# Kernel optimization log

Measured on AMD Instinct MI355X. Metric: run time of the kernel, lower is better.

Reference implementation:

```python
import jax, jax.numpy as jnp
import numpy as np

N = 100000        # nodes
E = 1600000       # edges
G = 128           # graphs in batch
D_FEAT = 240      # continuous node features (input_features - 1)
EMB = 16          # node-type embedding dim
H = 256           # hidden size (both layers)
PH = 128          # pool / classifier hidden
GF = 32           # global feature dim
LN_EPS = 1e-5


def setup_inputs() -> dict:
    key = jax.random.key(0)
    ks = jax.random.split(key, 24)

    node_types = jax.random.randint(ks[0], (N,), 0, 400).astype(jnp.float32)
    feats = jax.random.normal(ks[1], (N, D_FEAT), dtype=jnp.float32)
    x = jnp.concatenate([node_types[:, None], feats], axis=1)  # [N, 241]

    edge_index = jax.random.randint(ks[2], (2, E), 0, N, dtype=jnp.int32)
    batch = jnp.sort(jax.random.randint(ks[3], (N,), 0, G, dtype=jnp.int32))
    global_features = jax.random.normal(ks[4], (G, GF), dtype=jnp.float32)

    s = 0.05
    p = {}
    p['emb_table'] = jax.random.normal(ks[5], (400, EMB), dtype=jnp.float32) * s
    # layer 0 GIN MLP (in=256 -> 256 -> 256) + LayerNorm
    p['l0_w1'] = jax.random.normal(ks[6], (H, H), dtype=jnp.float32) * s
    p['l0_b1'] = jnp.zeros((H,), jnp.float32)
    p['l0_w2'] = jax.random.normal(ks[7], (H, H), dtype=jnp.float32) * s
    p['l0_b2'] = jnp.zeros((H,), jnp.float32)
    p['ln0_g'] = jnp.ones((H,), jnp.float32)
    p['ln0_b'] = jnp.zeros((H,), jnp.float32)
    # layer 1
    p['l1_w1'] = jax.random.normal(ks[8], (H, H), dtype=jnp.float32) * s
    p['l1_b1'] = jnp.zeros((H,), jnp.float32)
    p['l1_w2'] = jax.random.normal(ks[9], (H, H), dtype=jnp.float32) * s
    p['l1_b2'] = jnp.zeros((H,), jnp.float32)
    p['ln1_g'] = jnp.ones((H,), jnp.float32)
    p['ln1_b'] = jnp.zeros((H,), jnp.float32)
    # attentional aggregation gate: 256 -> 128 -> 1
    p['gate_w1'] = jax.random.normal(ks[10], (H, PH), dtype=jnp.float32) * s
    p['gate_b1'] = jnp.zeros((PH,), jnp.float32)
    p['gate_w2'] = jax.random.normal(ks[11], (PH, 1), dtype=jnp.float32) * s
    p['gate_b2'] = jnp.zeros((1,), jnp.float32)
    # classifier: 256+32 -> 128 -> 2
    p['cls_w1'] = jax.random.normal(ks[12], (H + GF, PH), dtype=jnp.float32) * s
    p['cls_b1'] = jnp.zeros((PH,), jnp.float32)
    p['cls_w2'] = jax.random.normal(ks[13], (PH, 2), dtype=jnp.float32) * s
    p['cls_b2'] = jnp.zeros((2,), jnp.float32)

    return dict(x=x, edge_index=edge_index, batch=batch,
                global_features=global_features, **p)


def _layernorm(z, g, b):
    mu = jnp.mean(z, axis=-1, keepdims=True)
    var = jnp.mean(jnp.square(z - mu), axis=-1, keepdims=True)
    return (z - mu) * jax.lax.rsqrt(var + LN_EPS) * g + b


def _gin_block(h, src, dst, w1, b1, w2, b2, ln_g, ln_b):
    # GINConv, eps=0: mlp((1+eps)*x_i + sum_{j->i} x_j)
    agg = jax.ops.segment_sum(h[src], dst, num_segments=h.shape[0])
    z = h + agg
    z = jax.nn.relu(z @ w1 + b1) @ w2 + b2
    z = jax.nn.relu(_layernorm(z, ln_g, ln_b))
    return h + z  # dropout is identity in eval; residual


def reference(x, edge_index, batch, global_features, emb_table,
              l0_w1, l0_b1, l0_w2, l0_b2, ln0_g, ln0_b,
              l1_w1, l1_b1, l1_w2, l1_b2, ln1_g, ln1_b,
              gate_w1, gate_b1, gate_w2, gate_b2,
              cls_w1, cls_b1, cls_w2, cls_b2):
    node_types = x[:, 0].astype(jnp.int32)
    h = jnp.concatenate([x[:, 1:], emb_table[node_types]], axis=1)  # [N, 256]

    src, dst = edge_index[0], edge_index[1]
    h = _gin_block(h, src, dst, l0_w1, l0_b1, l0_w2, l0_b2, ln0_g, ln0_b)
    h = _gin_block(h, src, dst, l1_w1, l1_b1, l1_w2, l1_b2, ln1_g, ln1_b)

    # AttentionalAggregation: segment softmax over gate scores, weighted sum
    gate = jax.nn.relu(h @ gate_w1 + gate_b1) @ gate_w2 + gate_b2  # [N, 1]
    gate = gate[:, 0]
    m = jax.ops.segment_max(gate, batch, num_segments=G)
    a = jnp.exp(gate - m[batch])
    s = jax.ops.segment_sum(a, batch, num_segments=G)
    w = a / s[batch]
    pooled = jax.ops.segment_sum(w[:, None] * h, batch, num_segments=G)  # [G, 256]

    z = jnp.concatenate([pooled, global_features], axis=1)  # [G, 288]
    out = jax.nn.relu(z @ cls_w1 + cls_b1) @ cls_w2 + cls_b2  # [G, 2]
    return out
```

## Files before the change

### kernel.cpp

```cpp
#include <hip/hip_runtime.h>
#include <math.h>

#define N_NODES 100000
#define N_EDGES 1600000
#define NG      128
#define HD      256
#define PHD     128
#define GFD     32
#define XW      241
#define LN_EPS  1e-5f
#define SLOT    64

typedef __attribute__((ext_vector_type(8))) short bf8_t;
typedef __attribute__((ext_vector_type(4))) float f4_t;

static __device__ __forceinline__ float relu_f(float x){ return fmaxf(x, 0.0f); }

static __device__ __forceinline__ unsigned short f2bf_rn(float v) {
    unsigned int u = __float_as_uint(v);
    unsigned int r = (u + 0x7fffu + ((u >> 16) & 1u)) >> 16;
    return (unsigned short)r;
}
static __device__ __forceinline__ float bf2f(unsigned short h) {
    return __uint_as_float((unsigned int)h << 16);
}

__global__ void build_h_kernel(const float* __restrict__ x, const float* __restrict__ emb,
                               float* __restrict__ h, unsigned short* __restrict__ h16)
{
    int node = blockIdx.x;
    int tid  = threadIdx.x;
    const float* xr = x + (size_t)node * XW;
    float v;
    if (tid < 240) {
        v = xr[1 + tid];
    } else {
        int t = (int)xr[0];
        v = emb[t * 16 + (tid - 240)];
    }
    h[(size_t)node * HD + tid] = v;
    h16[(size_t)node * HD + tid] = f2bf_rn(v);
}

__global__ void fill_slots_kernel(const int* __restrict__ src, const int* __restrict__ dst,
                                  int* __restrict__ cnt, int* __restrict__ col, int e)
{
    int i = blockIdx.x * blockDim.x + threadIdx.x;
    if (i < e) {
        int d = dst[i];
        int p = atomicAdd(&cnt[d], 1);
        if (p < SLOT) col[(size_t)d * SLOT + p] = src[i];
    }
}

static __device__ __forceinline__ void pack_one(const float* __restrict__ w, short* __restrict__ hi,
                                                int N, int fbase)
{
    int lane = threadIdx.x & 63;
    int f = fbase * 4 + (threadIdx.x >> 6);
    const int KB = 8;
    int nb = f / KB, kb = f % KB;
    int n = nb * 16 + (lane & 15);
    int k0 = kb * 32 + (lane >> 4) * 8;
    size_t o = (size_t)f * 512 + lane * 8;
    #pragma unroll
    for (int j = 0; j < 8; j++) {
        float v = w[(size_t)(k0 + j) * N + n];
        hi[o + j] = (short)f2bf_rn(v);
    }
}

__global__ __launch_bounds__(256) void pack_all_kernel(
    const float* __restrict__ w0, const float* __restrict__ w1,
    const float* __restrict__ w2, const float* __restrict__ w3,
    const float* __restrict__ w4,
    short* o0h, short* o1h, short* o2h, short* o3h, short* o4h)
{
    int b = blockIdx.x;
    if      (b < 32)  pack_one(w0, o0h, HD,  b);
    else if (b < 64)  pack_one(w1, o1h, HD,  b - 32);
    else if (b < 96)  pack_one(w2, o2h, HD,  b - 64);
    else if (b < 128) pack_one(w3, o3h, HD,  b - 96);
    else              pack_one(w4, o4h, PHD, b - 128);
}

static __device__ __forceinline__ void mm32(
    f4_t (&acc)[2][4], const char* buf,
    const short* __restrict__ Bh,
    int wc, int cb, int kg, int lane)
{
    bf8_t bcur[4], bnxt[4];
    #pragma unroll
    for (int ni = 0; ni < 4; ni++)
        bcur[ni] = *(const bf8_t*)&Bh[((size_t)((wc*4+ni)*8))*512 + lane*8];
    for (int kb = 0; kb < 8; kb++) {
        if (kb < 7) {
            #pragma unroll
            for (int ni = 0; ni < 4; ni++)
                bnxt[ni] = *(const bf8_t*)&Bh[((size_t)((wc*4+ni)*8 + kb+1))*512 + lane*8];
        }
        bf8_t ahi[2], alo[2];
        #pragma unroll
        for (int mi = 0; mi < 2; mi++) {
            int row = mi*16 + cb;
            int byte = (row*512 + kb*64 + kg*16) ^ ((row & 7) << 4);
            ahi[mi] = *(const bf8_t*)(buf + byte);
            alo[mi] = *(const bf8_t*)(buf + 16384 + byte);
        }
        #pragma unroll
        for (int mi = 0; mi < 2; mi++)
            #pragma unroll
            for (int ni = 0; ni < 4; ni++)
                acc[mi][ni] = __builtin_amdgcn_mfma_f32_16x16x32_bf16(ahi[mi], bcur[ni], acc[mi][ni], 0, 0, 0);
        #pragma unroll
        for (int mi = 0; mi < 2; mi++)
            #pragma unroll
            for (int ni = 0; ni < 4; ni++)
                acc[mi][ni] = __builtin_amdgcn_mfma_f32_16x16x32_bf16(alo[mi], bcur[ni], acc[mi][ni], 0, 0, 0);
        #pragma unroll
        for (int ni = 0; ni < 4; ni++) bcur[ni] = bnxt[ni];
    }
}

__global__ __launch_bounds__(256, 4) void gin_layer_kernel(
    float* __restrict__ h, const unsigned short* __restrict__ h16i,
    unsigned short* __restrict__ h16o,
    const int* __restrict__ cnt, const int* __restrict__ col,
    const short* __restrict__ w1h, const float* __restrict__ b1,
    const short* __restrict__ w2h, const float* __restrict__ b2,
    const float* __restrict__ lng, const float* __restrict__ lnb)
{
    __shared__ char buf[32768];
    const int tid  = threadIdx.x;
    const int lane = tid & 63;
    const int wv   = tid >> 6;
    const int cb   = lane & 15;
    const int kg   = lane >> 4;
    const int l4   = lane * 4;
    const long row0 = (long)blockIdx.x * 32;

    for (int rr = 0; rr < 8; rr++) {
        int row = wv * 8 + rr;
        long grow = row0 + row;
        float4 a0 = *(const float4*)&h[grow * HD + l4];
        float4 a1 = make_float4(0,0,0,0), a2 = make_float4(0,0,0,0), a3 = make_float4(0,0,0,0);
        int deg = cnt[grow]; if (deg > SLOT) deg = SLOT;
        const int* cb4 = col + (size_t)grow * SLOT;
        int e = 0;
        for (; e + 4 <= deg; e += 4) {
            int s0 = cb4[e], s1 = cb4[e+1], s2 = cb4[e+2], s3 = cb4[e+3];
            ushort4 u0 = *(const ushort4*)&h16i[(size_t)s0 * HD + l4];
            ushort4 u1 = *(const ushort4*)&h16i[(size_t)s1 * HD + l4];
            ushort4 u2 = *(const ushort4*)&h16i[(size_t)s2 * HD + l4];
            ushort4 u3 = *(const ushort4*)&h16i[(size_t)s3 * HD + l4];
            a0.x += bf2f(u0.x); a0.y += bf2f(u0.y); a0.z += bf2f(u0.z); a0.w += bf2f(u0.w);
            a1.x += bf2f(u1.x); a1.y += bf2f(u1.y); a1.z += bf2f(u1.z); a1.w += bf2f(u1.w);
            a2.x += bf2f(u2.x); a2.y += bf2f(u2.y); a2.z += bf2f(u2.z); a2.w += bf2f(u2.w);
            a3.x += bf2f(u3.x); a3.y += bf2f(u3.y); a3.z += bf2f(u3.z); a3.w += bf2f(u3.w);
        }
        for (; e < deg; e++) {
            int s = cb4[e];
            ushort4 u = *(const ushort4*)&h16i[(size_t)s * HD + l4];
            a0.x += bf2f(u.x); a0.y += bf2f(u.y); a0.z += bf2f(u.z); a0.w += bf2f(u.w);
        }
        a0.x += a1.x + a2.x + a3.x;
        a0.y += a1.y + a2.y + a3.y;
        a0.z += a1.z + a2.z + a3.z;
        a0.w += a1.w + a2.w + a3.w;
        ushort4 hi4, lo4;
        unsigned short hb;
        hb = f2bf_rn(a0.x); hi4.x = hb; lo4.x = f2bf_rn(a0.x - bf2f(hb));
        hb = f2bf_rn(a0.y); hi4.y = hb; lo4.y = f2bf_rn(a0.y - bf2f(hb));
        hb = f2bf_rn(a0.z); hi4.z = hb; lo4.z = f2bf_rn(a0.z - bf2f(hb));
        hb = f2bf_rn(a0.w); hi4.w = hb; lo4.w = f2bf_rn(a0.w - bf2f(hb));
        int byte = (row * 512 + lane * 8) ^ ((row & 7) << 4);
        *(ushort4*)(buf + byte)         = hi4;
        *(ushort4*)(buf + 16384 + byte) = lo4;
    }
    __syncthreads();

    f4_t acc[2][4];
    const f4_t zero4 = {0.f, 0.f, 0.f, 0.f};
    #pragma unroll
    for (int mi = 0; mi < 2; mi++)
        #pragma unroll
        for (int ni = 0; ni < 4; ni++) acc[mi][ni] = zero4;

    mm32(acc, buf, w1h, wv, cb, kg, lane);
    __syncthreads();

    {
        float bias1[4];
        #pragma unroll
        for (int ni = 0; ni < 4; ni++) bias1[ni] = b1[wv * 64 + ni * 16 + cb];
        #pragma unroll
        for (int mi = 0; mi < 2; mi++) {
            #pragma unroll
            for (int ni = 0; ni < 4; ni++) {
                int colx2 = (wv * 64 + ni * 16 + cb) * 2;
                #pragma unroll
                for (int j = 0; j < 4; j++) {
                    float t = relu_f(acc[mi][ni][j] + bias1[ni]);
                    int row = mi * 16 + kg * 4 + j;
                    unsigned short hb = f2bf_rn(t);
                    unsigned short lb = f2bf_rn(t - bf2f(hb));
                    int byte = (row * 512 + colx2) ^ ((row & 7) << 4);
                    *(short*)(buf + byte)         = (short)hb;
                    *(short*)(buf + 16384 + byte) = (short)lb;
                }
            }
        }
    }
    __syncthreads();

    #pragma unroll
    for (int mi = 0; mi < 2; mi++)
        #pragma unroll
        for (int ni = 0; ni < 4; ni++) acc[mi][ni] = zero4;

    mm32(acc, buf, w2h, wv, cb, kg, lane);
    __syncthreads();

    {
        float bias2[4];
        #pragma unroll
        for (int ni = 0; ni < 4; ni++) bias2[ni] = b2[wv * 64 + ni * 16 + cb];
        #pragma unroll
        for (int mi = 0; mi < 2; mi++) {
            #pragma unroll
            for (int ni = 0; ni < 4; ni++) {
                int col2 = wv * 64 + ni * 16 + cb;
                #pragma unroll
                for (int j = 0; j < 4; j++) {
                    int row = mi * 16 + kg * 4 + j;
                    int byte = (row * 1024 + col2 * 4) ^ (((row >> 2) & 3) << 6);
                    *(float*)(buf + byte) = acc[mi][ni][j] + bias2[ni];
                }
            }
        }
    }
    __syncthreads();

    {
        const float4 gv = *(const float4*)&lng[l4];
        const float4 bv = *(const float4*)&lnb[l4];
        for (int rr = 0; rr < 8; rr++) {
            int row = wv * 8 + rr;
            long grow = row0 + row;
            int byte = (row * 1024 + lane * 16) ^ (((row >> 2) & 3) << 6);
            float4 v = *(const float4*)(buf + byte);
            float s = v.x + v.y + v.z + v.w;
            float q = v.x * v.x + v.y * v.y + v.z * v.z + v.w * v.w;
            #pragma unroll
            for (int off = 32; off > 0; off >>= 1) {
                s += __shfl_xor(s, off, 64);
                q += __shfl_xor(q, off, 64);
            }
            float mu = s * (1.0f / 256.0f);
            float var = q * (1.0f / 256.0f) - mu * mu;
            float rstd = rsqrtf(var + LN_EPS);
            size_t gi = (size_t)grow * HD + l4;
            float4 hv = *(float4*)&h[gi];
            hv.x += relu_f((v.x - mu) * rstd * gv.x + bv.x);
            hv.y += relu_f((v.y - mu) * rstd * gv.y + bv.y);
            hv.z += relu_f((v.z - mu) * rstd * gv.z + bv.z);
            hv.w += relu_f((v.w - mu) * rstd * gv.w + bv.w);
            *(float4*)&h[gi] = hv;
            ushort4 m16;
            m16.x = f2bf_rn(hv.x); m16.y = f2bf_rn(hv.y);
            m16.z = f2bf_rn(hv.z); m16.w = f2bf_rn(hv.w);
            *(ushort4*)&h16o[gi] = m16;
        }
    }
}

__global__ __launch_bounds__(256, 2) void gate_mfma_kernel(
    const float* __restrict__ h,
    const short* __restrict__ g1h, const float* __restrict__ gb1,
    const float* __restrict__ gw2, const float* __restrict__ gb2,
    float* __restrict__ gate)
{
    __shared__ char buf[65536];
    const int tid  = threadIdx.x;
    const int lane = tid & 63;
    const int wv   = tid >> 6;
    const int cb   = lane & 15;
    const int kg   = lane >> 4;
    const long row0 = (long)blockIdx.x * 64;

    for (int rr = 0; rr < 16; rr++) {
        int row = wv * 16 + rr;
        long grow = row0 + row;
        float4 v = make_float4(0.f, 0.f, 0.f, 0.f);
        if (grow < N_NODES) v = *(const float4*)&h[grow * HD + lane * 4];
        ushort4 hi4, lo4;
        unsigned short hb;
        hb = f2bf_rn(v.x); hi4.x = hb; lo4.x = f2bf_rn(v.x - bf2f(hb));
        hb = f2bf_rn(v.y); hi4.y = hb; lo4.y = f2bf_rn(v.y - bf2f(hb));
        hb = f2bf_rn(v.z); hi4.z = hb; lo4.z = f2bf_rn(v.z - bf2f(hb));
        hb = f2bf_rn(v.w); hi4.w = hb; lo4.w = f2bf_rn(v.w - bf2f(hb));
        int byte = (row * 512 + lane * 8) ^ ((row & 7) << 4);
        *(ushort4*)(buf + byte)         = hi4;
        *(ushort4*)(buf + 32768 + byte) = lo4;
    }
    __syncthreads();

    f4_t acc[4][2];
    const f4_t zero4 = {0.f, 0.f, 0.f, 0.f};
    #pragma unroll
    for (int mi = 0; mi < 4; mi++) { acc[mi][0] = zero4; acc[mi][1] = zero4; }

    #pragma unroll
    for (int pass = 0; pass < 2; pass++) {
        const char* Abase = (pass == 1) ? (buf + 32768) : buf;
        for (int kb = 0; kb < 8; kb++) {
            bf8_t a[4], b[2];
            #pragma unroll
            for (int mi = 0; mi < 4; mi++) {
                int row = mi * 16 + cb;
                int byte = (row * 512 + kb * 64 + kg * 16) ^ ((row & 7) << 4);
                a[mi] = *(const bf8_t*)(Abase + byte);
            }
            #pragma unroll
            for (int ni = 0; ni < 2; ni++) {
                int nb = wv * 2 + ni;
                b[ni] = *(const bf8_t*)&g1h[(size_t)(nb * 8 + kb) * 512 + lane * 8];
            }
            #pragma unroll
            for (int mi = 0; mi < 4; mi++)
                #pragma unroll
                for (int ni = 0; ni < 2; ni++)
                    acc[mi][ni] = __builtin_amdgcn_mfma_f32_16x16x32_bf16(a[mi], b[ni], acc[mi][ni], 0, 0, 0);
        }
    }
    __syncthreads();

    {
        float* G1 = (float*)buf;
        float bias1[2];
        bias1[0] = gb1[wv * 32 + cb];
        bias1[1] = gb1[wv * 32 + 16 + cb];
        #pragma unroll
        for (int mi = 0; mi < 4; mi++) {
            #pragma unroll
            for (int ni = 0; ni < 2; ni++) {
                int colv = wv * 32 + ni * 16 + cb;
                #pragma unroll
                for (int j = 0; j < 4; j++) {
                    int row = mi * 16 + kg * 4 + j;
                    G1[row * PHD + colv] = relu_f(acc[mi][ni][j] + bias1[ni]);
                }
            }
        }
    }
    __syncthreads();

    {
        const float* G1 = (const float*)buf;
        float2 wv2 = *(const float2*)&gw2[lane * 2];
        float b2v = gb2[0];
        for (int rr = 0; rr < 16; rr++) {
            int row = wv * 16 + rr;
            long grow = row0 + row;
            if (grow >= N_NODES) break;
            float2 t2 = *(const float2*)&G1[row * PHD + lane * 2];
            float p = t2.x * wv2.x + t2.y * wv2.y;
            #pragma unroll
            for (int off = 32; off > 0; off >>= 1) p += __shfl_xor(p, off, 64);
            if (lane == 0) gate[grow] = p + b2v;
        }
    }
}

__global__ void goff_kernel(const int* __restrict__ batch, int* __restrict__ goff, int n)
{
    int t = threadIdx.x;
    if (t > NG) return;
    int lo = 0, hi = n;
    while (lo < hi) {
        int mid = (lo + hi) >> 1;
        if (batch[mid] < t) lo = mid + 1; else hi = mid;
    }
    goff[t] = lo;
}

__global__ __launch_bounds__(256) void pool_kernel(
    const float* __restrict__ h, const float* __restrict__ gate,
    const int* __restrict__ goff, float* __restrict__ pooled)
{
    __shared__ float red[256];
    __shared__ float m_sh, s_sh;
    int g = blockIdx.x >> 2, q = blockIdx.x & 3;
    int tid = threadIdx.x;
    int beg = goff[g], end = goff[g + 1];
    if (beg >= end) return;

    float lm = -3.4e38f;
    for (int i = beg + tid; i < end; i += 256) lm = fmaxf(lm, gate[i]);
    red[tid] = lm; __syncthreads();
    for (int off = 128; off > 0; off >>= 1) {
        if (tid < off) red[tid] = fmaxf(red[tid], red[tid + off]);
        __syncthreads();
    }
    if (tid == 0) m_sh = red[0];
    __syncthreads();
    float m = m_sh;

    float ls = 0.0f;
    for (int i = beg + tid; i < end; i += 256) ls += expf(gate[i] - m);
    __syncthreads();
    red[tid] = ls; __syncthreads();
    for (int off = 128; off > 0; off >>= 1) {
        if (tid < off) red[tid] += red[tid + off];
        __syncthreads();
    }
    if (tid == 0) s_sh = red[0];
    __syncthreads();
    float inv_s = 1.0f / s_sh;

    float acc = 0.0f;
    for (int i = beg + q; i < end; i += 4) {
        float a = expf(gate[i] - m);
        acc += a * h[(size_t)i * HD + tid];
    }
    atomicAdd(&pooled[(size_t)g * HD + tid], acc * inv_s);
}

__global__ __launch_bounds__(128) void cls_kernel(
    const float* __restrict__ pooled, const float* __restrict__ gf,
    const float* __restrict__ w1, const float* __restrict__ b1,
    const float* __restrict__ w2, const float* __restrict__ b2,
    float* __restrict__ out)
{
    __shared__ float r0[128], r1[128];
    int g = blockIdx.x, c = threadIdx.x;
    float acc = b1[c];
    const float* pr = pooled + (size_t)g * HD;
    for (int k = 0; k < HD; k++) acc += pr[k] * w1[k * PHD + c];
    const float* gr = gf + g * GFD;
    for (int k = 0; k < GFD; k++) acc += gr[k] * w1[(HD + k) * PHD + c];
    float t = relu_f(acc);
    r0[c] = t * w2[c * 2 + 0];
    r1[c] = t * w2[c * 2 + 1];
    __syncthreads();
    for (int off = 64; off > 0; off >>= 1) {
        if (c < off) { r0[c] += r0[c + off]; r1[c] += r1[c + off]; }
        __syncthreads();
    }
    if (c == 0) {
        out[g * 2 + 0] = r0[0] + b2[0];
        out[g * 2 + 1] = r1[0] + b2[1];
    }
}

extern "C" void kernel_launch(void* const* d_in, const int* in_sizes, int n_in,
                              void* d_out, int out_size, void* d_ws, size_t ws_size,
                              hipStream_t stream)
{
    const float* x    = (const float*)d_in[0];
    const int*   ei   = (const int*)d_in[1];
    const int*   bat  = (const int*)d_in[2];
    const float* gf   = (const float*)d_in[3];
    const float* emb  = (const float*)d_in[4];
    const float* l0w1 = (const float*)d_in[5];
    const float* l0b1 = (const float*)d_in[6];
    const float* l0w2 = (const float*)d_in[7];
    const float* l0b2 = (const float*)d_in[8];
    const float* ln0g = (const float*)d_in[9];
    const float* ln0b = (const float*)d_in[10];
    const float* l1w1 = (const float*)d_in[11];
    const float* l1b1 = (const float*)d_in[12];
    const float* l1w2 = (const float*)d_in[13];
    const float* l1b2 = (const float*)d_in[14];
    const float* ln1g = (const float*)d_in[15];
    const float* ln1b = (const float*)d_in[16];
    const float* gw1  = (const float*)d_in[17];
    const float* gb1  = (const float*)d_in[18];
    const float* gw2  = (const float*)d_in[19];
    const float* gb2  = (const float*)d_in[20];
    const float* cw1  = (const float*)d_in[21];
    const float* cb1  = (const float*)d_in[22];
    const float* cw2  = (const float*)d_in[23];
    const float* cb2  = (const float*)d_in[24];

    char* ws = (char*)d_ws;
    size_t off = 0;
    auto alloc = [&](size_t bytes) {
        void* p = ws + off;
        off += (bytes + 255) & ~(size_t)255;
        return p;
    };
    float* h      = (float*)alloc((size_t)N_NODES * HD * 4);
    unsigned short* h16a = (unsigned short*)alloc((size_t)N_NODES * HD * 2);
    unsigned short* h16b = (unsigned short*)alloc((size_t)N_NODES * HD * 2);
    float* gate   = (float*)alloc((size_t)N_NODES * 4);
    int*   cnt    = (int*)alloc((size_t)N_NODES * 4);
    int*   col    = (int*)alloc((size_t)N_NODES * SLOT * 4);
    int*   goff   = (int*)alloc((NG + 1) * 4);
    float* pooled = (float*)alloc((size_t)NG * HD * 4);
    short* p_l0w1h = (short*)alloc((size_t)HD * HD * 2);
    short* p_l0w2h = (short*)alloc((size_t)HD * HD * 2);
    short* p_l1w1h = (short*)alloc((size_t)HD * HD * 2);
    short* p_l1w2h = (short*)alloc((size_t)HD * HD * 2);
    short* p_gw1h  = (short*)alloc((size_t)HD * PHD * 2);

    const int* src = ei;
    const int* dst = ei + N_EDGES;

    build_h_kernel<<<N_NODES, 256, 0, stream>>>(x, emb, h, h16a);

    hipMemsetAsync(cnt, 0, (size_t)N_NODES * 4, stream);
    fill_slots_kernel<<<(N_EDGES + 255) / 256, 256, 0, stream>>>(src, dst, cnt, col, N_EDGES);

    pack_all_kernel<<<144, 256, 0, stream>>>(l0w1, l0w2, l1w1, l1w2, gw1,
                                             p_l0w1h, p_l0w2h, p_l1w1h, p_l1w2h, p_gw1h);

    const int layer_grid = N_NODES / 32;

    gin_layer_kernel<<<layer_grid, 256, 0, stream>>>(h, h16a, h16b, cnt, col,
                                                     p_l0w1h, l0b1, p_l0w2h, l0b2, ln0g, ln0b);
    gin_layer_kernel<<<layer_grid, 256, 0, stream>>>(h, h16b, h16a, cnt, col,
                                                     p_l1w1h, l1b1, p_l1w2h, l1b2, ln1g, ln1b);

    gate_mfma_kernel<<<(N_NODES + 63) / 64, 256, 0, stream>>>(h, p_gw1h, gb1, gw2, gb2, gate);
    goff_kernel<<<1, 256, 0, stream>>>(bat, goff, N_NODES);
    hipMemsetAsync(pooled, 0, (size_t)NG * HD * 4, stream);
    pool_kernel<<<NG * 4, 256, 0, stream>>>(h, gate, goff, pooled);
    cls_kernel<<<NG, 128, 0, stream>>>(pooled, gf, cw1, cb1, cw2, cb2, (float*)d_out);
}
```

Baseline: 769.7 us.

## Merge prep kernels into one launch and use bf16 single-pass gate GEMM

Three setup kernels (edge slot filling, input h construction, weight packing) are merged into one prep kernel whose block ranges pick the task, removing launch gaps. The col writes now use nontemporal stores. The gate kernel reads the already-available bf16 copy of h and drops the hi/lo split-bf16 second MFMA pass, halving gate GEMM work and the fp32 h read. This lowers gate-score precision to plain bf16, which may affect tolerance.

```diff
diff --git a/kernel.cpp b/kernel.cpp
--- a/kernel.cpp
+++ b/kernel.cpp
@@ -10,6 +10,8 @@
 #define XW      241
 #define LN_EPS  1e-5f
 #define SLOT    64
+#define EDGE_NB ((N_EDGES + 255) / 256)
+#define PACK_NB 144
 
 typedef __attribute__((ext_vector_type(8))) short bf8_t;
 typedef __attribute__((ext_vector_type(4))) float f4_t;
@@ -23,34 +25,6 @@
 }
 static __device__ __forceinline__ float bf2f(unsigned short h) {
     return __uint_as_float((unsigned int)h << 16);
-}
-
-__global__ void build_h_kernel(const float* __restrict__ x, const float* __restrict__ emb,
-                               float* __restrict__ h, unsigned short* __restrict__ h16)
-{
-    int node = blockIdx.x;
-    int tid  = threadIdx.x;
-    const float* xr = x + (size_t)node * XW;
-    float v;
-    if (tid < 240) {
-        v = xr[1 + tid];
-    } else {
-        int t = (int)xr[0];
-        v = emb[t * 16 + (tid - 240)];
-    }
-    h[(size_t)node * HD + tid] = v;
-    h16[(size_t)node * HD + tid] = f2bf_rn(v);
-}
-
-__global__ void fill_slots_kernel(const int* __restrict__ src, const int* __restrict__ dst,
-                                  int* __restrict__ cnt, int* __restrict__ col, int e)
-{
-    int i = blockIdx.x * blockDim.x + threadIdx.x;
-    if (i < e) {
-        int d = dst[i];
-        int p = atomicAdd(&cnt[d], 1);
-        if (p < SLOT) col[(size_t)d * SLOT + p] = src[i];
-    }
 }
 
 static __device__ __forceinline__ void pack_one(const float* __restrict__ w, short* __restrict__ hi,
@@ -70,18 +44,45 @@
     }
 }
 
-__global__ __launch_bounds__(256) void pack_all_kernel(
+__global__ __launch_bounds__(256) void prep_kernel(
+    const float* __restrict__ x, const float* __restrict__ emb,
+    float* __restrict__ h, unsigned short* __restrict__ h16,
+    const int* __restrict__ src, const int* __restrict__ dst,
+    int* __restrict__ cnt, int* __restrict__ col,
     const float* __restrict__ w0, const float* __restrict__ w1,
     const float* __restrict__ w2, const float* __restrict__ w3,
     const float* __restrict__ w4,
     short* o0h, short* o1h, short* o2h, short* o3h, short* o4h)
 {
     int b = blockIdx.x;
-    if      (b < 32)  pack_one(w0, o0h, HD,  b);
-    else if (b < 64)  pack_one(w1, o1h, HD,  b - 32);
-    else if (b < 96)  pack_one(w2, o2h, HD,  b - 64);
-    else if (b < 128) pack_one(w3, o3h, HD,  b - 96);
-    else              pack_one(w4, o4h, PHD, b - 128);
+    int tid = threadIdx.x;
+    if (b < EDGE_NB) {
+        int i = b * 256 + tid;
+        if (i < N_EDGES) {
+            int d = dst[i];
+            int p = atomicAdd(&cnt[d], 1);
+            if (p < SLOT) __builtin_nontemporal_store(src[i], &col[(size_t)d * SLOT + p]);
+        }
+    } else if (b < EDGE_NB + N_NODES) {
+        int node = b - EDGE_NB;
+        const float* xr = x + (size_t)node * XW;
+        float v;
+        if (tid < 240) {
+            v = xr[1 + tid];
+        } else {
+            int t = (int)xr[0];
+            v = emb[t * 16 + (tid - 240)];
+        }
+        h[(size_t)node * HD + tid] = v;
+        h16[(size_t)node * HD + tid] = f2bf_rn(v);
+    } else {
+        int bb = b - EDGE_NB - N_NODES;
+        if      (bb < 32)  pack_one(w0, o0h, HD,  bb);
+        else if (bb < 64)  pack_one(w1, o1h, HD,  bb - 32);
+        else if (bb < 96)  pack_one(w2, o2h, HD,  bb - 64);
+        else if (bb < 128) pack_one(w3, o3h, HD,  bb - 96);
+        else               pack_one(w4, o4h, PHD, bb - 128);
+    }
 }
 
 static __device__ __forceinline__ void mm32(
@@ -275,7 +276,7 @@
 }
 
 __global__ __launch_bounds__(256, 2) void gate_mfma_kernel(
-    const float* __restrict__ h,
+    const unsigned short* __restrict__ h16,
     const short* __restrict__ g1h, const float* __restrict__ gb1,
     const float* __restrict__ gw2, const float* __restrict__ gb2,
     float* __restrict__ gate)
@@ -291,17 +292,10 @@
     for (int rr = 0; rr < 16; rr++) {
         int row = wv * 16 + rr;
         long grow = row0 + row;
-        float4 v = make_float4(0.f, 0.f, 0.f, 0.f);
-        if (grow < N_NODES) v = *(const float4*)&h[grow * HD + lane * 4];
-        ushort4 hi4, lo4;
-        unsigned short hb;
-        hb = f2bf_rn(v.x); hi4.x = hb; lo4.x = f2bf_rn(v.x - bf2f(hb));
-        hb = f2bf_rn(v.y); hi4.y = hb; lo4.y = f2bf_rn(v.y - bf2f(hb));
-        hb = f2bf_rn(v.z); hi4.z = hb; lo4.z = f2bf_rn(v.z - bf2f(hb));
-        hb = f2bf_rn(v.w); hi4.w = hb; lo4.w = f2bf_rn(v.w - bf2f(hb));
+        ushort4 u = make_ushort4(0, 0, 0, 0);
+        if (grow < N_NODES) u = *(const ushort4*)&h16[grow * HD + lane * 4];
         int byte = (row * 512 + lane * 8) ^ ((row & 7) << 4);
-        *(ushort4*)(buf + byte)         = hi4;
-        *(ushort4*)(buf + 32768 + byte) = lo4;
+        *(ushort4*)(buf + byte) = u;
     }
     __syncthreads();
 
@@ -310,28 +304,24 @@
     #pragma unroll
     for (int mi = 0; mi < 4; mi++) { acc[mi][0] = zero4; acc[mi][1] = zero4; }
 
-    #pragma unroll
-    for (int pass = 0; pass < 2; pass++) {
-        const char* Abase = (pass == 1) ? (buf + 32768) : buf;
-        for (int kb = 0; kb < 8; kb++) {
-            bf8_t a[4], b[2];
-            #pragma unroll
-            for (int mi = 0; mi < 4; mi++) {
-                int row = mi * 16 + cb;
-                int byte = (row * 512 + kb * 64 + kg * 16) ^ ((row & 7) << 4);
-                a[mi] = *(const bf8_t*)(Abase + byte);
-            }
-            #pragma unroll
-            for (int ni = 0; ni < 2; ni++) {
-                int nb = wv * 2 + ni;
-                b[ni] = *(const bf8_t*)&g1h[(size_t)(nb * 8 + kb) * 512 + lane * 8];
-            }
-            #pragma unroll
-            for (int mi = 0; mi < 4; mi++)
-                #pragma unroll
-                for (int ni = 0; ni < 2; ni++)
-                    acc[mi][ni] = __builtin_amdgcn_mfma_f32_16x16x32_bf16(a[mi], b[ni], acc[mi][ni], 0, 0, 0);
-        }
+    for (int kb = 0; kb < 8; kb++) {
+        bf8_t a[4], b[2];
+        #pragma unroll
+        for (int mi = 0; mi < 4; mi++) {
+            int row = mi * 16 + cb;
+            int byte = (row * 512 + kb * 64 + kg * 16) ^ ((row & 7) << 4);
+            a[mi] = *(const bf8_t*)(buf + byte);
+        }
+        #pragma unroll
+        for (int ni = 0; ni < 2; ni++) {
+            int nb = wv * 2 + ni;
+            b[ni] = *(const bf8_t*)&g1h[(size_t)(nb * 8 + kb) * 512 + lane * 8];
+        }
+        #pragma unroll
+        for (int mi = 0; mi < 4; mi++)
+            #pragma unroll
+            for (int ni = 0; ni < 2; ni++)
+                acc[mi][ni] = __builtin_amdgcn_mfma_f32_16x16x32_bf16(a[mi], b[ni], acc[mi][ni], 0, 0, 0);
     }
     __syncthreads();
 
@@ -507,13 +497,11 @@
     const int* src = ei;
     const int* dst = ei + N_EDGES;
 
-    build_h_kernel<<<N_NODES, 256, 0, stream>>>(x, emb, h, h16a);
-
     hipMemsetAsync(cnt, 0, (size_t)N_NODES * 4, stream);
-    fill_slots_kernel<<<(N_EDGES + 255) / 256, 256, 0, stream>>>(src, dst, cnt, col, N_EDGES);
-
-    pack_all_kernel<<<144, 256, 0, stream>>>(l0w1, l0w2, l1w1, l1w2, gw1,
-                                             p_l0w1h, p_l0w2h, p_l1w1h, p_l1w2h, p_gw1h);
+    prep_kernel<<<EDGE_NB + N_NODES + PACK_NB, 256, 0, stream>>>(
+        x, emb, h, h16a, src, dst, cnt, col,
+        l0w1, l0w2, l1w1, l1w2, gw1,
+        p_l0w1h, p_l0w2h, p_l1w1h, p_l1w2h, p_gw1h);
 
     const int layer_grid = N_NODES / 32;
 
@@ -522,7 +510,7 @@
     gin_layer_kernel<<<layer_grid, 256, 0, stream>>>(h, h16b, h16a, cnt, col,
                                                      p_l1w1h, l1b1, p_l1w2h, l1b2, ln1g, ln1b);
 
-    gate_mfma_kernel<<<(N_NODES + 63) / 64, 256, 0, stream>>>(h, p_gw1h, gb1, gw2, gb2, gate);
+    gate_mfma_kernel<<<(N_NODES + 63) / 64, 256, 0, stream>>>(h16a, p_gw1h, gb1, gw2, gb2, gate);
     goff_kernel<<<1, 256, 0, stream>>>(bat, goff, N_NODES);
     hipMemsetAsync(pooled, 0, (size_t)NG * HD * 4, stream);
     pool_kernel<<<NG * 4, 256, 0, stream>>>(h, gate, goff, pooled);
```

New measurement: 801.6 us. +4.1%, slower.
